# Kernel optimization log

Hardware: AMD Instinct MI355X
Metric: run time of the kernel (lower is better)

The kernel has to match this reference:

```python
import jax, jax.numpy as jnp
import numpy as np

N = 100000
E = 1600000
D_IN = 128
D_OUT = 128


def setup_inputs() -> dict:
    key = jax.random.key(0)
    ks = jax.random.split(key, 6)
    seq = jax.random.normal(ks[0], (N, D_IN), dtype=jnp.float32)
    edge_src = jax.random.randint(ks[1], (E,), 0, N, dtype=jnp.int32)
    edge_dst = jax.random.randint(ks[2], (E,), 0, N, dtype=jnp.int32)
    adj_vals = jax.random.uniform(ks[3], (E,), dtype=jnp.float32)
    # xavier_uniform for [out, in] -> stored as [in, out] for x @ W
    lim = float(np.sqrt(6.0 / (D_IN + D_OUT)))
    w_fc = jax.random.uniform(ks[4], (D_IN, D_OUT), jnp.float32, -lim, lim)
    w_proj = jax.random.uniform(ks[5], (D_IN, D_OUT), jnp.float32, -lim, lim)
    b_proj = jnp.zeros((D_OUT,), jnp.float32)
    bias = jnp.zeros((D_OUT,), jnp.float32)
    return {"seq": seq, "edge_src": edge_src, "edge_dst": edge_dst,
            "adj_vals": adj_vals, "w_fc": w_fc, "w_proj": w_proj,
            "b_proj": b_proj, "bias": bias}


def reference(seq, edge_src, edge_dst, adj_vals, w_fc, w_proj, b_proj, bias):
    # h = fc(seq)  (no bias)
    h = seq @ w_fc                                  # [N, D_OUT]
    # spmm(adj, h): out[i] = sum_{e: dst=i} vals[e] * h[src[e]]
    msgs = adj_vals[:, None] * h[edge_src]          # [E, D_OUT]
    agg = jax.ops.segment_sum(msgs, edge_dst, num_segments=N)
    # bias add + residual proj(seq) add + tanh
    out = jnp.tanh(agg + bias + seq @ w_proj + b_proj)
    return out
```

## Files before the change

kernel.cpp:

```cpp
#include <hip/hip_runtime.h>
#include <math.h>


typedef __attribute__((ext_vector_type(8))) short short8;
typedef __attribute__((ext_vector_type(4))) float float4v;
typedef __attribute__((ext_vector_type(2))) _Float16 half2v;

#define PG 256
#define NBMAX 2048

static __device__ __forceinline__ short f2bf(float x) {
    unsigned u = __float_as_uint(x);
    unsigned r = (u + 0x7fffu + ((u >> 16) & 1u)) >> 16;
    return (short)r;
}
static __device__ __forceinline__ float bf2f(short h) {
    return __uint_as_float(((unsigned)(unsigned short)h) << 16);
}

__global__ __launch_bounds__(256)
void wconv_kernel(const float* __restrict__ wa, const float* __restrict__ wb,
                  short* __restrict__ whia, short* __restrict__ wloa,
                  short* __restrict__ whib, short* __restrict__ wlob) {
    const int bb = blockIdx.x;
    const float* w  = (bb < 16) ? wa   : wb;
    short* whi      = (bb < 16) ? whia : whib;
    short* wlo      = (bb < 16) ? wloa : wlob;
    const int i = (bb & 15) * 256 + threadIdx.x;
    const float4 v = ((const float4*)w)[i];
    const int k = i >> 5;
    const int c4 = (i & 31) * 4;
    float xs[4] = {v.x, v.y, v.z, v.w};
    #pragma unroll
    for (int j = 0; j < 4; j++) {
        const short hi = f2bf(xs[j]);
        const short lo = f2bf(xs[j] - bf2f(hi));
        whi[(c4 + j) * 128 + k] = hi;
        wlo[(c4 + j) * 128 + k] = lo;
    }
}

#define KP 136

__global__ __launch_bounds__(256, 2)
void mm_mfma_kernel(const float* __restrict__ seq, const short* __restrict__ whi,
                    const short* __restrict__ wlo,
                    const float* __restrict__ b0p, const float* __restrict__ b1p,
                    float* __restrict__ out, _Float16* __restrict__ out16,
                    int N, int add_bias) {
    __shared__ short wt_hi[128 * KP];
    __shared__ short wt_lo[128 * KP];

    const int tid = threadIdx.x;
    for (int i = tid; i < 2048; i += 256) {
        const int row = i >> 4;
        const int k8  = (i & 15) * 8;
        *(float4*)&wt_hi[row * KP + k8] = ((const float4*)whi)[i];
        *(float4*)&wt_lo[row * KP + k8] = ((const float4*)wlo)[i];
    }
    __syncthreads();

    const int wave = tid >> 6;
    const int lane = tid & 63;
    const int q = lane >> 4;
    const int c = lane & 15;
    const int R = blockIdx.x * 64 + wave * 16;
    const int rowL = (R + c < N) ? (R + c) : (N - 1);

    float4v acc[8];
    #pragma unroll
    for (int ct = 0; ct < 8; ct++) acc[ct] = (float4v){0.f, 0.f, 0.f, 0.f};

    #pragma unroll
    for (int t = 0; t < 4; t++) {
        const int kk = t * 32 + q * 8;
        const float4 a0 = *(const float4*)&seq[(size_t)rowL * 128 + kk];
        const float4 a1 = *(const float4*)&seq[(size_t)rowL * 128 + kk + 4];
        float xs[8] = {a0.x, a0.y, a0.z, a0.w, a1.x, a1.y, a1.z, a1.w};
        union { short s[8]; short8 v; } ahi, alo;
        #pragma unroll
        for (int j = 0; j < 8; j++) {
            const short hi = f2bf(xs[j]);
            ahi.s[j] = hi;
            alo.s[j] = f2bf(xs[j] - bf2f(hi));
        }
        #pragma unroll
        for (int ct = 0; ct < 8; ct++) {
            const int n = ct * 16 + c;
            const short8 bhi = *(const short8*)&wt_hi[n * KP + kk];
            const short8 blo = *(const short8*)&wt_lo[n * KP + kk];
            acc[ct] = __builtin_amdgcn_mfma_f32_16x16x32_bf16(ahi.v, bhi, acc[ct], 0, 0, 0);
            acc[ct] = __builtin_amdgcn_mfma_f32_16x16x32_bf16(ahi.v, blo, acc[ct], 0, 0, 0);
            acc[ct] = __builtin_amdgcn_mfma_f32_16x16x32_bf16(alo.v, bhi, acc[ct], 0, 0, 0);
        }
    }

    if (out16) {
        #pragma unroll
        for (int ct = 0; ct < 8; ct++) {
            const int col = ct * 16 + c;
            #pragma unroll
            for (int r = 0; r < 4; r++) {
                const int row = R + q * 4 + r;
                if (row < N) out16[(size_t)row * 128 + col] = (_Float16)acc[ct][r];
            }
        }
    } else {
        #pragma unroll
        for (int ct = 0; ct < 8; ct++) {
            const int col = ct * 16 + c;
            float badd = 0.f;
            if (add_bias) badd = b0p[col] + b1p[col];
            #pragma unroll
            for (int r = 0; r < 4; r++) {
                const int row = R + q * 4 + r;
                if (row < N) out[(size_t)row * 128 + col] = acc[ct][r] + badd;
            }
        }
    }
}


__global__ __launch_bounds__(256)
void phist_kernel(const int* __restrict__ edst, int* __restrict__ hcnt,
                  int E, int S, int NB) {
    __shared__ int cnt[NBMAX];
    const int g = blockIdx.x;
    const int tid = threadIdx.x;
    for (int b = tid; b < NB; b += 256) cnt[b] = 0;
    __syncthreads();
    const int lo = g * S;
    const int hi = (lo + S < E) ? (lo + S) : E;
    for (int i = lo + tid; i < hi; i += 256)
        atomicAdd(&cnt[edst[i] >> 6], 1);
    __syncthreads();
    for (int b = tid; b < NB; b += 256) hcnt[b * PG + g] = cnt[b];
}

__global__ __launch_bounds__(256)
void pscan1_kernel(const int* __restrict__ in, int* __restrict__ out,
                   int* __restrict__ bsum, int L) {
    __shared__ int s[256];
    const int t = threadIdx.x;
    const int base = blockIdx.x * 2048 + t * 8;
    int v[8];
    int mysum = 0;
    #pragma unroll
    for (int j = 0; j < 8; j++) {
        v[j] = (base + j < L) ? in[base + j] : 0;
        mysum += v[j];
    }
    s[t] = mysum;
    __syncthreads();
    for (int o = 1; o < 256; o <<= 1) {
        int add = (t >= o) ? s[t - o] : 0;
        __syncthreads();
        s[t] += add;
        __syncthreads();
    }
    int run = s[t] - mysum;
    #pragma unroll
    for (int j = 0; j < 8; j++) {
        if (base + j < L) out[base + j] = run;
        run += v[j];
    }
    if (t == 255) bsum[blockIdx.x] = s[255];
}

__global__ __launch_bounds__(256)
void pscan2_kernel(const int* __restrict__ bsum, int* __restrict__ ebsum, int nb) {
    __shared__ int s[256];
    const int t = threadIdx.x;
    const int v = (t < nb) ? bsum[t] : 0;
    s[t] = v;
    __syncthreads();
    for (int o = 1; o < 256; o <<= 1) {
        int add = (t >= o) ? s[t - o] : 0;
        __syncthreads();
        s[t] += add;
        __syncthreads();
    }
    if (t < nb) ebsum[t] = s[t] - v;
}

__global__ __launch_bounds__(256)
void paddback_kernel(int* __restrict__ pos, const int* __restrict__ ebsum,
                     int* __restrict__ bstart, int L, int NB, int E) {
    const int add = ebsum[blockIdx.x];
    const int base = blockIdx.x * 2048 + threadIdx.x * 8;
    #pragma unroll
    for (int j = 0; j < 8; j++) {
        const int idx = base + j;
        if (idx < L) {
            const int v = pos[idx] + add;
            pos[idx] = v;
            if ((idx & (PG - 1)) == 0) bstart[idx / PG] = v;
        }
    }
    if (blockIdx.x == 0 && threadIdx.x == 0) bstart[NB] = E;
}

__global__ __launch_bounds__(256)
void pscatter_kernel(const int* __restrict__ esrc, const int* __restrict__ edst,
                     const float* __restrict__ vals, const int* __restrict__ pos,
                     int2* __restrict__ sedge, int E, int S, int NB) {
    __shared__ int cur[NBMAX];
    const int g = blockIdx.x;
    const int tid = threadIdx.x;
    for (int b = tid; b < NB; b += 256) cur[b] = pos[b * PG + g];
    __syncthreads();
    const int lo = g * S;
    const int hi = (lo + S < E) ? (lo + S) : E;
    for (int i = lo + tid; i < hi; i += 256) {
        const int d = edst[i];
        const int p = atomicAdd(&cur[d >> 6], 1);
        sedge[p] = make_int2((esrc[i] << 6) | (d & 63), __float_as_int(vals[i]));
    }
}

#define CAP 2048

__global__ __launch_bounds__(256, 8)
void aggregate_sorted(const int* __restrict__ bstart, const int2* __restrict__ sedge,
                      const _Float16* __restrict__ h, float* __restrict__ out, int N) {
    __shared__ int2 ebuf[CAP];
    __shared__ int cnt[64], sc[64], off[65], cur[64];
    const int b = blockIdx.x;
    const int tid = threadIdx.x;
    const int beg = bstart[b];
    const int total = bstart[b + 1] - beg;
    const int cl = total < CAP ? total : CAP;

    if (tid < 64) cnt[tid] = 0;
    __syncthreads();
    for (int i = tid; i < cl; i += 256)
        atomicAdd(&cnt[sedge[beg + i].x & 63], 1);
    __syncthreads();
    if (tid < 64) sc[tid] = cnt[tid];
    __syncthreads();
    for (int o = 1; o < 64; o <<= 1) {
        int add = (tid < 64 && tid >= o) ? sc[tid - o] : 0;
        __syncthreads();
        if (tid < 64) sc[tid] += add;
        __syncthreads();
    }
    if (tid < 64) { off[tid] = sc[tid] - cnt[tid]; cur[tid] = sc[tid] - cnt[tid]; }
    if (tid == 63) off[64] = sc[63];
    __syncthreads();
    for (int i = tid; i < cl; i += 256) {
        const int2 e = sedge[beg + i];
        const int p = atomicAdd(&cur[e.x & 63], 1);
        ebuf[p] = e;
    }
    __syncthreads();

    const int wave = tid >> 6;
    const int lane = tid & 63;
    const char* hb = (const char*)h;
    const int loff = lane << 2;

    for (int n = wave * 16; n < wave * 16 + 16; n++) {
        const int node = b * 64 + n;
        if (node >= N) break;
        float2 acc = make_float2(0.f, 0.f);
        const int e0 = off[n], e1 = off[n + 1];
        int j = e0;
        for (; j + 8 <= e1; j += 8) {
            const int2 e0v = ebuf[j],     e1v = ebuf[j + 1];
            const int2 e2v = ebuf[j + 2], e3v = ebuf[j + 3];
            const int2 e4v = ebuf[j + 4], e5v = ebuf[j + 5];
            const int2 e6v = ebuf[j + 6], e7v = ebuf[j + 7];
            const half2v h0 = *(const half2v*)(hb + ((((unsigned)e0v.x >> 6) << 8) + loff));
            const half2v h1 = *(const half2v*)(hb + ((((unsigned)e1v.x >> 6) << 8) + loff));
            const half2v h2 = *(const half2v*)(hb + ((((unsigned)e2v.x >> 6) << 8) + loff));
            const half2v h3 = *(const half2v*)(hb + ((((unsigned)e3v.x >> 6) << 8) + loff));
            const half2v h4 = *(const half2v*)(hb + ((((unsigned)e4v.x >> 6) << 8) + loff));
            const half2v h5 = *(const half2v*)(hb + ((((unsigned)e5v.x >> 6) << 8) + loff));
            const half2v h6 = *(const half2v*)(hb + ((((unsigned)e6v.x >> 6) << 8) + loff));
            const half2v h7 = *(const half2v*)(hb + ((((unsigned)e7v.x >> 6) << 8) + loff));
            const float v0 = __int_as_float(e0v.y), v1 = __int_as_float(e1v.y);
            const float v2 = __int_as_float(e2v.y), v3 = __int_as_float(e3v.y);
            const float v4 = __int_as_float(e4v.y), v5 = __int_as_float(e5v.y);
            const float v6 = __int_as_float(e6v.y), v7 = __int_as_float(e7v.y);
            acc.x += v0 * (float)h0.x; acc.y += v0 * (float)h0.y;
            acc.x += v1 * (float)h1.x; acc.y += v1 * (float)h1.y;
            acc.x += v2 * (float)h2.x; acc.y += v2 * (float)h2.y;
            acc.x += v3 * (float)h3.x; acc.y += v3 * (float)h3.y;
            acc.x += v4 * (float)h4.x; acc.y += v4 * (float)h4.y;
            acc.x += v5 * (float)h5.x; acc.y += v5 * (float)h5.y;
            acc.x += v6 * (float)h6.x; acc.y += v6 * (float)h6.y;
            acc.x += v7 * (float)h7.x; acc.y += v7 * (float)h7.y;
        }
        for (; j + 4 <= e1; j += 4) {
            const int2 ea = ebuf[j], eb = ebuf[j + 1], ec = ebuf[j + 2], ed = ebuf[j + 3];
            const half2v h0 = *(const half2v*)(hb + ((((unsigned)ea.x >> 6) << 8) + loff));
            const half2v h1 = *(const half2v*)(hb + ((((unsigned)eb.x >> 6) << 8) + loff));
            const half2v h2 = *(const half2v*)(hb + ((((unsigned)ec.x >> 6) << 8) + loff));
            const half2v h3 = *(const half2v*)(hb + ((((unsigned)ed.x >> 6) << 8) + loff));
            const float v0 = __int_as_float(ea.y), v1 = __int_as_float(eb.y);
            const float v2 = __int_as_float(ec.y), v3 = __int_as_float(ed.y);
            acc.x += v0 * (float)h0.x; acc.y += v0 * (float)h0.y;
            acc.x += v1 * (float)h1.x; acc.y += v1 * (float)h1.y;
            acc.x += v2 * (float)h2.x; acc.y += v2 * (float)h2.y;
            acc.x += v3 * (float)h3.x; acc.y += v3 * (float)h3.y;
        }
        for (; j < e1; j++) {
            const int2 e = ebuf[j];
            const float v = __int_as_float(e.y);
            const half2v hv = *(const half2v*)(hb + ((((unsigned)e.x >> 6) << 8) + loff));
            acc.x += v * (float)hv.x; acc.y += v * (float)hv.y;
        }
        for (int t2 = cl; t2 < total; t2++) {
            const int2 e = sedge[beg + t2];
            if ((e.x & 63) == n) {
                const float v = __int_as_float(e.y);
                const half2v hv = *(const half2v*)(hb + ((((unsigned)e.x >> 6) << 8) + loff));
                acc.x += v * (float)hv.x; acc.y += v * (float)hv.y;
            }
        }
        union { double d; float2 f; } bv, rv;
        const double* op = (const double*)out + (size_t)node * 64 + lane;
        bv.d = __builtin_nontemporal_load(op);
        rv.f.x = tanhf(acc.x + bv.f.x);
        rv.f.y = tanhf(acc.y + bv.f.y);
        __builtin_nontemporal_store(rv.d, (double*)out + (size_t)node * 64 + lane);
    }
}


__global__ __launch_bounds__(256)
void edge_scatter(const int* __restrict__ esrc, const int* __restrict__ edst,
                  const float* __restrict__ vals, const _Float16* __restrict__ h,
                  float* __restrict__ out, int E) {
    const int gtid = blockIdx.x * blockDim.x + threadIdx.x;
    const int wave = gtid >> 6;
    const int lane = threadIdx.x & 63;
    const int nw = (gridDim.x * blockDim.x) >> 6;
    for (int e = wave; e < E; e += nw) {
        const int s = esrc[e];
        const int d = edst[e];
        const float v = vals[e];
        const half2v hv = *(const half2v*)(h + (size_t)s * 128 + lane * 2);
        float* op = out + (size_t)d * 128 + lane * 2;
        atomicAdd(op, v * (float)hv.x);
        atomicAdd(op + 1, v * (float)hv.y);
    }
}

__global__ __launch_bounds__(256)
void tanh_kernel(float* __restrict__ out, int n4) {
    const int i = blockIdx.x * blockDim.x + threadIdx.x;
    if (i < n4) {
        float4 v = ((float4*)out)[i];
        v.x = tanhf(v.x);
        v.y = tanhf(v.y);
        v.z = tanhf(v.z);
        v.w = tanhf(v.w);
        ((float4*)out)[i] = v;
    }
}

static inline size_t align64(size_t x) { return (x + 63) & ~(size_t)63; }

extern "C" void kernel_launch(void* const* d_in, const int* in_sizes, int n_in,
                              void* d_out, int out_size, void* d_ws, size_t ws_size,
                              hipStream_t stream) {
    const float* seq    = (const float*)d_in[0];
    const int*   esrc   = (const int*)  d_in[1];
    const int*   edst   = (const int*)  d_in[2];
    const float* vals   = (const float*)d_in[3];
    const float* w_fc   = (const float*)d_in[4];
    const float* w_proj = (const float*)d_in[5];
    const float* b_proj = (const float*)d_in[6];
    const float* bias   = (const float*)d_in[7];
    float* out = (float*)d_out;

    const int N = in_sizes[0] / 128;
    const int E = in_sizes[1];
    const int NB = (N + 63) >> 6;
    const int L  = NB * PG;
    const int S  = (E + PG - 1) / PG;
    const int nsb = (L + 2047) / 2048;

    char* ws = (char*)d_ws;
    const size_t o_h     = 0;
    const size_t o_whif  = align64(o_h    + (size_t)N * 128 * 2);
    const size_t o_wlof  = align64(o_whif + 32768);
    const size_t o_whip  = align64(o_wlof + 32768);
    const size_t o_wlop  = align64(o_whip + 32768);
    const size_t o_hc    = align64(o_wlop + 32768);
    const size_t o_pos   = align64(o_hc   + (size_t)L * 4);
    const size_t o_bs    = align64(o_pos  + (size_t)L * 4);
    const size_t o_bsum  = align64(o_bs   + (size_t)(NB + 1) * 4);
    const size_t o_ebs   = align64(o_bsum + 1024);
    const size_t o_sed   = align64(o_ebs  + 1024);
    const size_t need    = o_sed + (size_t)E * 8;

    _Float16* h   = (_Float16*)(ws + o_h);
    short* whi_fc = (short*)(ws + o_whif);
    short* wlo_fc = (short*)(ws + o_wlof);
    short* whi_pj = (short*)(ws + o_whip);
    short* wlo_pj = (short*)(ws + o_wlop);
    int*   hcnt   = (int*)  (ws + o_hc);
    int*   pos    = (int*)  (ws + o_pos);
    int*   bstart = (int*)  (ws + o_bs);
    int*   bsum   = (int*)  (ws + o_bsum);
    int*   ebsum  = (int*)  (ws + o_ebs);
    int2*  sedge  = (int2*) (ws + o_sed);

    const int mm_blocks = (N + 63) / 64;

    wconv_kernel<<<32, 256, 0, stream>>>(w_fc, w_proj, whi_fc, wlo_fc, whi_pj, wlo_pj);
    mm_mfma_kernel<<<mm_blocks, 256, 0, stream>>>(seq, whi_fc, wlo_fc, nullptr, nullptr, nullptr, h, N, 0);
    mm_mfma_kernel<<<mm_blocks, 256, 0, stream>>>(seq, whi_pj, wlo_pj, b_proj, bias, out, nullptr, N, 1);

    if (ws_size >= need && NB <= NBMAX && nsb <= 256) {
        phist_kernel<<<PG, 256, 0, stream>>>(edst, hcnt, E, S, NB);
        pscan1_kernel<<<nsb, 256, 0, stream>>>(hcnt, pos, bsum, L);
        pscan2_kernel<<<1, 256, 0, stream>>>(bsum, ebsum, nsb);
        paddback_kernel<<<nsb, 256, 0, stream>>>(pos, ebsum, bstart, L, NB, E);
        pscatter_kernel<<<PG, 256, 0, stream>>>(esrc, edst, vals, pos, sedge, E, S, NB);
        aggregate_sorted<<<NB, 256, 0, stream>>>(bstart, sedge, h, out, N);
    } else {
        edge_scatter<<<8192, 256, 0, stream>>>(esrc, edst, vals, h, out, E);
        const int n4 = (N * 128) / 4;
        tanh_kernel<<<(n4 + 255) / 256, 256, 0, stream>>>(out, n4);
    }
}
```

Measured before the change: 324.7 us.

## Persistent grid for MFMA matmul and 4-edge-per-wave 16B gathers in aggregation

```diff
diff --git a/kernel.cpp b/kernel.cpp
--- a/kernel.cpp
+++ b/kernel.cpp
@@ -47,7 +47,7 @@
                     const short* __restrict__ wlo,
                     const float* __restrict__ b0p, const float* __restrict__ b1p,
                     float* __restrict__ out, _Float16* __restrict__ out16,
-                    int N, int add_bias) {
+                    int N, int add_bias, int ntiles) {
     __shared__ short wt_hi[128 * KP];
     __shared__ short wt_lo[128 * KP];
 
@@ -64,57 +64,60 @@
     const int lane = tid & 63;
     const int q = lane >> 4;
     const int c = lane & 15;
-    const int R = blockIdx.x * 64 + wave * 16;
-    const int rowL = (R + c < N) ? (R + c) : (N - 1);
-
-    float4v acc[8];
-    #pragma unroll
-    for (int ct = 0; ct < 8; ct++) acc[ct] = (float4v){0.f, 0.f, 0.f, 0.f};
-
-    #pragma unroll
-    for (int t = 0; t < 4; t++) {
-        const int kk = t * 32 + q * 8;
-        const float4 a0 = *(const float4*)&seq[(size_t)rowL * 128 + kk];
-        const float4 a1 = *(const float4*)&seq[(size_t)rowL * 128 + kk + 4];
-        float xs[8] = {a0.x, a0.y, a0.z, a0.w, a1.x, a1.y, a1.z, a1.w};
-        union { short s[8]; short8 v; } ahi, alo;
+
+    for (int tile = blockIdx.x; tile < ntiles; tile += gridDim.x) {
+        const int R = tile * 64 + wave * 16;
+        const int rowL = (R + c < N) ? (R + c) : (N - 1);
+
+        float4v acc[8];
         #pragma unroll
-        for (int j = 0; j < 8; j++) {
-            const short hi = f2bf(xs[j]);
-            ahi.s[j] = hi;
-            alo.s[j] = f2bf(xs[j] - bf2f(hi));
+        for (int ct = 0; ct < 8; ct++) acc[ct] = (float4v){0.f, 0.f, 0.f, 0.f};
+
+        #pragma unroll
+        for (int t = 0; t < 4; t++) {
+            const int kk = t * 32 + q * 8;
+            const float4 a0 = *(const float4*)&seq[(size_t)rowL * 128 + kk];
+            const float4 a1 = *(const float4*)&seq[(size_t)rowL * 128 + kk + 4];
+            float xs[8] = {a0.x, a0.y, a0.z, a0.w, a1.x, a1.y, a1.z, a1.w};
+            union { short s[8]; short8 v; } ahi, alo;
+            #pragma unroll
+            for (int j = 0; j < 8; j++) {
+                const short hi = f2bf(xs[j]);
+                ahi.s[j] = hi;
+                alo.s[j] = f2bf(xs[j] - bf2f(hi));
+            }
+            #pragma unroll
+            for (int ct = 0; ct < 8; ct++) {
+                const int n = ct * 16 + c;
+                const short8 bhi = *(const short8*)&wt_hi[n * KP + kk];
+                const short8 blo = *(const short8*)&wt_lo[n * KP + kk];
+                acc[ct] = __builtin_amdgcn_mfma_f32_16x16x32_bf16(ahi.v, bhi, acc[ct], 0, 0, 0);
+                acc[ct] = __builtin_amdgcn_mfma_f32_16x16x32_bf16(ahi.v, blo, acc[ct], 0, 0, 0);
+                acc[ct] = __builtin_amdgcn_mfma_f32_16x16x32_bf16(alo.v, bhi, acc[ct], 0, 0, 0);
+            }
         }
-        #pragma unroll
-        for (int ct = 0; ct < 8; ct++) {
-            const int n = ct * 16 + c;
-            const short8 bhi = *(const short8*)&wt_hi[n * KP + kk];
-            const short8 blo = *(const short8*)&wt_lo[n * KP + kk];
-            acc[ct] = __builtin_amdgcn_mfma_f32_16x16x32_bf16(ahi.v, bhi, acc[ct], 0, 0, 0);
-            acc[ct] = __builtin_amdgcn_mfma_f32_16x16x32_bf16(ahi.v, blo, acc[ct], 0, 0, 0);
-            acc[ct] = __builtin_amdgcn_mfma_f32_16x16x32_bf16(alo.v, bhi, acc[ct], 0, 0, 0);
-        }
-    }
-
-    if (out16) {
-        #pragma unroll
-        for (int ct = 0; ct < 8; ct++) {
-            const int col = ct * 16 + c;
+
+        if (out16) {
             #pragma unroll
-            for (int r = 0; r < 4; r++) {
-                const int row = R + q * 4 + r;
-                if (row < N) out16[(size_t)row * 128 + col] = (_Float16)acc[ct][r];
-            }
-        }
-    } else {
-        #pragma unroll
-        for (int ct = 0; ct < 8; ct++) {
-            const int col = ct * 16 + c;
-            float badd = 0.f;
-            if (add_bias) badd = b0p[col] + b1p[col];
+            for (int ct = 0; ct < 8; ct++) {
+                const int col = ct * 16 + c;
+                #pragma unroll
+                for (int r = 0; r < 4; r++) {
+                    const int row = R + q * 4 + r;
+                    if (row < N) out16[(size_t)row * 128 + col] = (_Float16)acc[ct][r];
+                }
+            }
+        } else {
             #pragma unroll
-            for (int r = 0; r < 4; r++) {
-                const int row = R + q * 4 + r;
-                if (row < N) out[(size_t)row * 128 + col] = acc[ct][r] + badd;
+            for (int ct = 0; ct < 8; ct++) {
+                const int col = ct * 16 + c;
+                float badd = 0.f;
+                if (add_bias) badd = b0p[col] + b1p[col];
+                #pragma unroll
+                for (int r = 0; r < 4; r++) {
+                    const int row = R + q * 4 + r;
+                    if (row < N) out[(size_t)row * 128 + col] = acc[ct][r] + badd;
+                }
             }
         }
     }
@@ -256,74 +259,76 @@
 
     const int wave = tid >> 6;
     const int lane = tid & 63;
+    const int g = lane >> 4;
+    const int c = lane & 15;
     const char* hb = (const char*)h;
-    const int loff = lane << 2;
+    const unsigned coff = (unsigned)c << 4;
 
     for (int n = wave * 16; n < wave * 16 + 16; n++) {
         const int node = b * 64 + n;
         if (node >= N) break;
-        float2 acc = make_float2(0.f, 0.f);
         const int e0 = off[n], e1 = off[n + 1];
-        int j = e0;
-        for (; j + 8 <= e1; j += 8) {
-            const int2 e0v = ebuf[j],     e1v = ebuf[j + 1];
-            const int2 e2v = ebuf[j + 2], e3v = ebuf[j + 3];
-            const int2 e4v = ebuf[j + 4], e5v = ebuf[j + 5];
-            const int2 e6v = ebuf[j + 6], e7v = ebuf[j + 7];
-            const half2v h0 = *(const half2v*)(hb + ((((unsigned)e0v.x >> 6) << 8) + loff));
-            const half2v h1 = *(const half2v*)(hb + ((((unsigned)e1v.x >> 6) << 8) + loff));
-            const half2v h2 = *(const half2v*)(hb + ((((unsigned)e2v.x >> 6) << 8) + loff));
-            const half2v h3 = *(const half2v*)(hb + ((((unsigned)e3v.x >> 6) << 8) + loff));
-            const half2v h4 = *(const half2v*)(hb + ((((unsigned)e4v.x >> 6) << 8) + loff));
-            const half2v h5 = *(const half2v*)(hb + ((((unsigned)e5v.x >> 6) << 8) + loff));
-            const half2v h6 = *(const half2v*)(hb + ((((unsigned)e6v.x >> 6) << 8) + loff));
-            const half2v h7 = *(const half2v*)(hb + ((((unsigned)e7v.x >> 6) << 8) + loff));
-            const float v0 = __int_as_float(e0v.y), v1 = __int_as_float(e1v.y);
-            const float v2 = __int_as_float(e2v.y), v3 = __int_as_float(e3v.y);
-            const float v4 = __int_as_float(e4v.y), v5 = __int_as_float(e5v.y);
-            const float v6 = __int_as_float(e6v.y), v7 = __int_as_float(e7v.y);
-            acc.x += v0 * (float)h0.x; acc.y += v0 * (float)h0.y;
-            acc.x += v1 * (float)h1.x; acc.y += v1 * (float)h1.y;
-            acc.x += v2 * (float)h2.x; acc.y += v2 * (float)h2.y;
-            acc.x += v3 * (float)h3.x; acc.y += v3 * (float)h3.y;
-            acc.x += v4 * (float)h4.x; acc.y += v4 * (float)h4.y;
-            acc.x += v5 * (float)h5.x; acc.y += v5 * (float)h5.y;
-            acc.x += v6 * (float)h6.x; acc.y += v6 * (float)h6.y;
-            acc.x += v7 * (float)h7.x; acc.y += v7 * (float)h7.y;
-        }
-        for (; j + 4 <= e1; j += 4) {
-            const int2 ea = ebuf[j], eb = ebuf[j + 1], ec = ebuf[j + 2], ed = ebuf[j + 3];
-            const half2v h0 = *(const half2v*)(hb + ((((unsigned)ea.x >> 6) << 8) + loff));
-            const half2v h1 = *(const half2v*)(hb + ((((unsigned)eb.x >> 6) << 8) + loff));
-            const half2v h2 = *(const half2v*)(hb + ((((unsigned)ec.x >> 6) << 8) + loff));
-            const half2v h3 = *(const half2v*)(hb + ((((unsigned)ed.x >> 6) << 8) + loff));
-            const float v0 = __int_as_float(ea.y), v1 = __int_as_float(eb.y);
-            const float v2 = __int_as_float(ec.y), v3 = __int_as_float(ed.y);
-            acc.x += v0 * (float)h0.x; acc.y += v0 * (float)h0.y;
-            acc.x += v1 * (float)h1.x; acc.y += v1 * (float)h1.y;
-            acc.x += v2 * (float)h2.x; acc.y += v2 * (float)h2.y;
-            acc.x += v3 * (float)h3.x; acc.y += v3 * (float)h3.y;
-        }
-        for (; j < e1; j++) {
-            const int2 e = ebuf[j];
-            const float v = __int_as_float(e.y);
-            const half2v hv = *(const half2v*)(hb + ((((unsigned)e.x >> 6) << 8) + loff));
-            acc.x += v * (float)hv.x; acc.y += v * (float)hv.y;
+        float a0 = 0.f, a1 = 0.f, a2 = 0.f, a3 = 0.f;
+        float a4 = 0.f, a5 = 0.f, a6 = 0.f, a7 = 0.f;
+
+        if (e1 > e0) {
+            int jj = e0 + g;
+            int2 eA = ebuf[jj < e1 ? jj : e0];
+            float vA = (jj < e1) ? __int_as_float(eA.y) : 0.f;
+            int4 hA = *(const int4*)(hb + ((((unsigned)eA.x >> 6) << 8) + coff));
+            for (int j = e0;;) {
+                const int jn = j + 4;
+                const bool more = jn < e1;
+                int2 eB; float vB = 0.f; int4 hB;
+                if (more) {
+                    const int j2 = jn + g;
+                    eB = ebuf[j2 < e1 ? j2 : e0];
+                    vB = (j2 < e1) ? __int_as_float(eB.y) : 0.f;
+                    hB = *(const int4*)(hb + ((((unsigned)eB.x >> 6) << 8) + coff));
+                }
+                union { int4 i4; half2v h2[4]; } u; u.i4 = hA;
+                a0 += vA * (float)u.h2[0].x; a1 += vA * (float)u.h2[0].y;
+                a2 += vA * (float)u.h2[1].x; a3 += vA * (float)u.h2[1].y;
+                a4 += vA * (float)u.h2[2].x; a5 += vA * (float)u.h2[2].y;
+                a6 += vA * (float)u.h2[3].x; a7 += vA * (float)u.h2[3].y;
+                if (!more) break;
+                hA = hB; vA = vB; j = jn;
+            }
         }
         for (int t2 = cl; t2 < total; t2++) {
             const int2 e = sedge[beg + t2];
             if ((e.x & 63) == n) {
-                const float v = __int_as_float(e.y);
-                const half2v hv = *(const half2v*)(hb + ((((unsigned)e.x >> 6) << 8) + loff));
-                acc.x += v * (float)hv.x; acc.y += v * (float)hv.y;
+                const float v = (g == 0) ? __int_as_float(e.y) : 0.f;
+                union { int4 i4; half2v h2[4]; } u;
+                u.i4 = *(const int4*)(hb + ((((unsigned)e.x >> 6) << 8) + coff));
+                a0 += v * (float)u.h2[0].x; a1 += v * (float)u.h2[0].y;
+                a2 += v * (float)u.h2[1].x; a3 += v * (float)u.h2[1].y;
+                a4 += v * (float)u.h2[2].x; a5 += v * (float)u.h2[2].y;
+                a6 += v * (float)u.h2[3].x; a7 += v * (float)u.h2[3].y;
             }
         }
+
+        a0 += __shfl_xor(a0, 16, 64); a0 += __shfl_xor(a0, 32, 64);
+        a1 += __shfl_xor(a1, 16, 64); a1 += __shfl_xor(a1, 32, 64);
+        a2 += __shfl_xor(a2, 16, 64); a2 += __shfl_xor(a2, 32, 64);
+        a3 += __shfl_xor(a3, 16, 64); a3 += __shfl_xor(a3, 32, 64);
+        a4 += __shfl_xor(a4, 16, 64); a4 += __shfl_xor(a4, 32, 64);
+        a5 += __shfl_xor(a5, 16, 64); a5 += __shfl_xor(a5, 32, 64);
+        a6 += __shfl_xor(a6, 16, 64); a6 += __shfl_xor(a6, 32, 64);
+        a7 += __shfl_xor(a7, 16, 64); a7 += __shfl_xor(a7, 32, 64);
+
+        float wx, wy;
+        if (g == 0)      { wx = a0; wy = a1; }
+        else if (g == 1) { wx = a2; wy = a3; }
+        else if (g == 2) { wx = a4; wy = a5; }
+        else             { wx = a6; wy = a7; }
+
         union { double d; float2 f; } bv, rv;
-        const double* op = (const double*)out + (size_t)node * 64 + lane;
-        bv.d = __builtin_nontemporal_load(op);
-        rv.f.x = tanhf(acc.x + bv.f.x);
-        rv.f.y = tanhf(acc.y + bv.f.y);
-        __builtin_nontemporal_store(rv.d, (double*)out + (size_t)node * 64 + lane);
+        const size_t oidx = (size_t)node * 64 + (unsigned)(c * 4 + g);
+        bv.d = __builtin_nontemporal_load((const double*)out + oidx);
+        rv.f.x = tanhf(wx + bv.f.x);
+        rv.f.y = tanhf(wy + bv.f.y);
+        __builtin_nontemporal_store(rv.d, (double*)out + oidx);
     }
 }
 
@@ -408,11 +413,12 @@
     int*   ebsum  = (int*)  (ws + o_ebs);
     int2*  sedge  = (int2*) (ws + o_sed);
 
-    const int mm_blocks = (N + 63) / 64;
+    const int ntiles = (N + 63) / 64;
+    const int mm_grid = ntiles < 512 ? ntiles : 512;
 
     wconv_kernel<<<32, 256, 0, stream>>>(w_fc, w_proj, whi_fc, wlo_fc, whi_pj, wlo_pj);
-    mm_mfma_kernel<<<mm_blocks, 256, 0, stream>>>(seq, whi_fc, wlo_fc, nullptr, nullptr, nullptr, h, N, 0);
-    mm_mfma_kernel<<<mm_blocks, 256, 0, stream>>>(seq, whi_pj, wlo_pj, b_proj, bias, out, nullptr, N, 1);
+    mm_mfma_kernel<<<mm_grid, 256, 0, stream>>>(seq, whi_fc, wlo_fc, nullptr, nullptr, nullptr, h, N, 0, ntiles);
+    mm_mfma_kernel<<<mm_grid, 256, 0, stream>>>(seq, whi_pj, wlo_pj, b_proj, bias, out, nullptr, N, 1, ntiles);
 
     if (ws_size >= need && NB <= NBMAX && nsb <= 256) {
         phist_kernel<<<PG, 256, 0, stream>>>(edst, hcnt, E, S, NB);
```

After: 386.4 us. 1.19x slower.
